# Performance work log

Measured on AMD Instinct MI355X. Metric: run time of the kernel, lower is better.

The kernel has to match this reference:

```python
import jax, jax.numpy as jnp
import numpy as np

B, N, D = 256, 64, 512        # batch, num_patches, dim
H, DH = 8, 64                 # heads, dim_head
INNER = H * DH                # 512
SCALE = DH ** -0.5


def setup_inputs() -> dict:
    key = jax.random.key(0)
    k0, k1, k2, k3, k4 = jax.random.split(key, 5)
    s = 0.02
    return {
        "x": jax.random.normal(k0, (B, N, D), jnp.float32),
        "Wq": jax.random.normal(k1, (D, INNER), jnp.float32) * s,      # to_q (no bias)
        "Wkv": jax.random.normal(k2, (D, 2 * INNER), jnp.float32) * s,  # to_k_v (no bias)
        "Wout": jax.random.normal(k3, (INNER, D), jnp.float32) * s,     # to_out Linear weight
        "bout": jnp.zeros((D,), jnp.float32),                           # to_out Linear bias
        "Wspec": jax.random.normal(k4, (N, 3 * N), jnp.float32) * s,    # to_qkv_spec (no bias)
    }


def reference(x, Wq, Wkv, Wout, bout, Wspec):
    b, n, d = x.shape
    # --- center-token spatial attention ---
    median_idx = n // 2
    x_center = jnp.broadcast_to(x[:, median_idx:median_idx + 1, :], (b, n, d))
    q = (x_center @ Wq).reshape(b, n, H, DH).transpose(0, 2, 1, 3)   # b h n dh
    kv = x @ Wkv                                                      # b n 2*inner
    k, v = jnp.split(kv, 2, axis=-1)
    k = k.reshape(b, n, H, DH).transpose(0, 2, 1, 3)                  # b h n dh
    v = v.reshape(b, n, H, DH).transpose(0, 2, 1, 3)                  # b h n dh
    attn = jax.nn.softmax(jnp.einsum('bhnd,bhmd->bhnm', q, k) * SCALE, axis=-1)
    out = jnp.einsum('bhnm,bhmd->bhnd', attn, v)                      # b h n dh
    out = out.transpose(0, 2, 1, 3).reshape(b, n, INNER)              # b n inner
    spatial_out = out @ Wout + bout                                   # b n d (dropout=0 -> identity)
    # --- transposed spectral attention ---
    x_t = x.transpose(0, 2, 1)                                        # b d n
    qkv = x_t @ Wspec                                                 # b d 3n
    q_s, k_s, _v_s = jnp.split(qkv, 3, axis=-1)                       # v_spec is unused in the original
    spec_weights = jax.nn.softmax(
        jnp.einsum('bdn,ben->bde', q_s, k_s) * SCALE, axis=-1)        # b d d
    # --- final combining matmul ---
    return jnp.einsum('bnd,bde->bne', spatial_out, spec_weights)      # b n d
```

## Files before the change

kernel.cpp:

```cpp
#include <hip/hip_runtime.h>

#define NP 64
#define DIM 512
#define NH 8
#define SCALE 0.125f

typedef __attribute__((ext_vector_type(4))) float f32x4;
typedef __attribute__((ext_vector_type(8))) short bf16x8;

#define WS_C   0
#define WS_MT  8192
#define WS_PT  4202496
#define WS_U   8396800
#define WS_Y   10493952

static __device__ __forceinline__ unsigned short f2bf(float f) {
  unsigned int u = __builtin_bit_cast(unsigned int, f);
  u += 0x7fffu + ((u >> 16) & 1u);
  return (unsigned short)(u >> 16);
}
static __device__ __forceinline__ float bf2f(unsigned short s) {
  return __builtin_bit_cast(float, ((unsigned int)s) << 16);
}
static __device__ __forceinline__ unsigned pk2(float a, float b) {
  return (unsigned)f2bf(a) | ((unsigned)f2bf(b) << 16);
}

__global__ __launch_bounds__(512)
void kw_prep(const float* __restrict__ Wq, const float* __restrict__ Wkv,
             const float* __restrict__ Wout, const float* __restrict__ Wspec,
             char* __restrict__ ws) {
  __shared__ float wa[64 * 65];
  __shared__ float wb[64 * 65];
  const int t = threadIdx.x;
  const int blk = blockIdx.x;
  const int sr = t >> 3, sc8 = (t & 7) * 8;

  if (blk == 1024) {
    #pragma unroll
    for (int cc = 0; cc < 8; ++cc) {
      wa[sr * 65 + sc8 + cc] = Wspec[sr * 192 + sc8 + cc];
      wb[sr * 65 + sc8 + cc] = Wspec[sr * 192 + 64 + sc8 + cc];
    }
    __syncthreads();
    const int m = sr, mm0 = sc8;
    float acc[8] = {0.f, 0.f, 0.f, 0.f, 0.f, 0.f, 0.f, 0.f};
    for (int n = 0; n < 64; ++n) {
      float qv = wa[m * 65 + n];
      #pragma unroll
      for (int j = 0; j < 8; ++j)
        acc[j] = fmaf(qv, wb[(mm0 + j) * 65 + n], acc[j]);
    }
    uint4 pk;
    pk.x = pk2(acc[0] * SCALE, acc[1] * SCALE);
    pk.y = pk2(acc[2] * SCALE, acc[3] * SCALE);
    pk.z = pk2(acc[4] * SCALE, acc[5] * SCALE);
    pk.w = pk2(acc[6] * SCALE, acc[7] * SCALE);
    *(uint4*)(ws + WS_C + m * 128 + ((mm0 * 2) ^ ((m & 7) << 4))) = pk;
    return;
  }

  const bool isP = blk >= 512;
  const int id = blk & 511;
  const int h = id >> 6, et = (id >> 3) & 7, dt = id & 7;

  const float* sa = isP ? (Wkv + (size_t)(dt * 64 + sr) * 1024 + 512 + h * 64)
                        : (Wq + (size_t)(dt * 64 + sr) * 512 + h * 64);
  const float* sb = isP ? (Wout + (size_t)(h * 64 + sr) * 512 + et * 64)
                        : (Wkv + (size_t)(et * 64 + sr) * 1024 + h * 64);
  {
    float4 a0 = *(const float4*)(sa + sc8), a1 = *(const float4*)(sa + sc8 + 4);
    float* d = wa + sr * 65 + sc8;
    d[0] = a0.x; d[1] = a0.y; d[2] = a0.z; d[3] = a0.w;
    d[4] = a1.x; d[5] = a1.y; d[6] = a1.z; d[7] = a1.w;
    float4 b0 = *(const float4*)(sb + sc8), b1 = *(const float4*)(sb + sc8 + 4);
    float* e = wb + sr * 65 + sc8;
    e[0] = b0.x; e[1] = b0.y; e[2] = b0.z; e[3] = b0.w;
    e[4] = b1.x; e[5] = b1.y; e[6] = b1.z; e[7] = b1.w;
  }
  __syncthreads();

  const int er = sr, dc8 = sc8;
  float acc[8] = {0.f, 0.f, 0.f, 0.f, 0.f, 0.f, 0.f, 0.f};
  if (!isP) {
    for (int j = 0; j < 64; ++j) {
      float bv = wb[er * 65 + j];
      #pragma unroll
      for (int dd = 0; dd < 8; ++dd)
        acc[dd] = fmaf(bv, wa[(dc8 + dd) * 65 + j], acc[dd]);
    }
  } else {
    for (int j = 0; j < 64; ++j) {
      float bv = wb[j * 65 + er];
      #pragma unroll
      for (int dd = 0; dd < 8; ++dd)
        acc[dd] = fmaf(bv, wa[(dc8 + dd) * 65 + j], acc[dd]);
    }
  }
  uint4 pk;
  pk.x = pk2(acc[0], acc[1]);
  pk.y = pk2(acc[2], acc[3]);
  pk.z = pk2(acc[4], acc[5]);
  pk.w = pk2(acc[6], acc[7]);
  if (!isP)
    *(uint4*)(ws + WS_MT + ((size_t)(h * 512 + et * 64 + er) * 512 + dt * 64 + dc8) * 2) = pk;
  else
    *(uint4*)(ws + WS_PT + ((size_t)(et * 64 + er) * 4096 + h * 512 + dt * 64 + dc8) * 2) = pk;
}

#define GEMM_LDS 131072
__global__ __launch_bounds__(512, 2)
void ku_u(const float* __restrict__ x, const char* __restrict__ ws,
          char* __restrict__ ws_u) {
  extern __shared__ char sm[];
  char* At = sm;
  char* Bt = sm + 65536;
  const int t = threadIdx.x, lane = t & 63, wave = t >> 6;
  const int bt = blockIdx.x >> 6, nt = blockIdx.x & 63;
  const int b0 = bt * 64, n0 = nt * 64;
  const char* Mt = ws + WS_MT;

  #pragma unroll
  for (int i = 0; i < 8; ++i) {
    const int r = wave * 8 + i;
    const float4* xr = (const float4*)(x + ((size_t)(b0 + r) * 64 + 32) * 512);
    float4 a = xr[lane], c = xr[64 + lane];
    uint2 pa = {pk2(a.x, a.y), pk2(a.z, a.w)};
    uint2 pc = {pk2(c.x, c.y), pk2(c.z, c.w)};
    const int swz = (r & 7) << 4;
    const int byt = (8 * (lane & 15)) ^ swz;
    *(uint2*)(At + (lane >> 4) * 8192 + r * 128 + byt) = pa;
    *(uint2*)(At + (4 + (lane >> 4)) * 8192 + r * 128 + byt) = pc;
  }
  #pragma unroll
  for (int i = 0; i < 8; ++i) {
    const int r = wave * 8 + i;
    uint4 v = ((const uint4*)(Mt + (size_t)(n0 + r) * 1024))[lane];
    *(uint4*)(Bt + (lane >> 3) * 8192 + r * 128 + ((16 * (lane & 7)) ^ ((r & 7) << 4))) = v;
  }
  __syncthreads();

  const int lo = ((lane & 15) * 128) + (((lane >> 4) * 16) ^ ((lane & 7) << 4));
  const int hi = ((lane & 15) * 128) + ((((lane >> 4) * 16) + 64) ^ ((lane & 7) << 4));
  const int bsub = wave & 3, npair = wave >> 2;

  f32x4 c0 = {0.f, 0.f, 0.f, 0.f}, c1 = {0.f, 0.f, 0.f, 0.f};
  #pragma unroll
  for (int kc = 0; kc < 8; ++kc) {
    const char* ab = At + kc * 8192 + bsub * 2048;
    bf16x8 aL = *(const bf16x8*)(ab + lo);
    bf16x8 aH = *(const bf16x8*)(ab + hi);
    const char* bb0 = Bt + kc * 8192 + (npair * 2) * 2048;
    const char* bb1 = bb0 + 2048;
    c0 = __builtin_amdgcn_mfma_f32_16x16x32_bf16(aL, *(const bf16x8*)(bb0 + lo), c0, 0, 0, 0);
    c0 = __builtin_amdgcn_mfma_f32_16x16x32_bf16(aH, *(const bf16x8*)(bb0 + hi), c0, 0, 0, 0);
    c1 = __builtin_amdgcn_mfma_f32_16x16x32_bf16(aL, *(const bf16x8*)(bb1 + lo), c1, 0, 0, 0);
    c1 = __builtin_amdgcn_mfma_f32_16x16x32_bf16(aH, *(const bf16x8*)(bb1 + hi), c1, 0, 0, 0);
  }
  unsigned short* U = (unsigned short*)ws_u;
  const int brow = b0 + bsub * 16 + (lane >> 4) * 4;
  const int nc0 = n0 + (npair * 2) * 16 + (lane & 15);
  #pragma unroll
  for (int r = 0; r < 4; ++r) {
    U[(size_t)(brow + r) * 4096 + nc0] = f2bf(c0[r]);
    U[(size_t)(brow + r) * 4096 + nc0 + 16] = f2bf(c1[r]);
  }
}

__global__ __launch_bounds__(512)
void k2_attn(const float* __restrict__ x, const char* __restrict__ ws_u,
             char* __restrict__ ws_y) {
  __shared__ float ul[8 * 512];
  __shared__ float scoreL[8 * 64];
  __shared__ float pT[64 * 8];
  const int t = threadIdx.x;
  const int lane = t & 63;
  const int wave = t >> 6;
  const int b = blockIdx.x;
  const float* xb = x + (size_t)b * NP * DIM;

  {
    uint4 v = ((const uint4*)(ws_u + (size_t)b * 8192))[t];
    const unsigned short* pv = (const unsigned short*)&v;
    float* d = ul + t * 8;
    #pragma unroll
    for (int g = 0; g < 8; ++g) d[g] = bf2f(pv[g]);
  }
  __syncthreads();

  {
    float4 uf0[8], uf1[8];
    #pragma unroll
    for (int h = 0; h < 8; ++h) {
      uf0[h] = *(const float4*)(ul + h * 512 + 4 * lane);
      uf1[h] = *(const float4*)(ul + h * 512 + 256 + 4 * lane);
    }
    #pragma unroll 2
    for (int i = 0; i < 8; ++i) {
      const int m = wave * 8 + i;
      const float4* xr = (const float4*)(xb + (size_t)m * DIM);
      float4 xv0 = xr[lane];
      float4 xv1 = xr[64 + lane];
      #pragma unroll
      for (int h = 0; h < 8; ++h) {
        float p = xv0.x * uf0[h].x + xv0.y * uf0[h].y + xv0.z * uf0[h].z + xv0.w * uf0[h].w
                + xv1.x * uf1[h].x + xv1.y * uf1[h].y + xv1.z * uf1[h].z + xv1.w * uf1[h].w;
        p += __shfl_xor(p, 1);
        p += __shfl_xor(p, 2);
        p += __shfl_xor(p, 4);
        p += __shfl_xor(p, 8);
        p += __shfl_xor(p, 16);
        p += __shfl_xor(p, 32);
        if (lane == 0) scoreL[h * 64 + m] = p;
      }
    }
  }
  __syncthreads();

  {
    float sc = scoreL[wave * 64 + lane] * SCALE;
    float mx = sc;
    #pragma unroll
    for (int off = 32; off > 0; off >>= 1)
      mx = fmaxf(mx, __shfl_xor(mx, off));
    float ev = __expf(sc - mx);
    float sm = ev;
    #pragma unroll
    for (int off = 32; off > 0; off >>= 1)
      sm += __shfl_xor(sm, off);
    pT[lane * NH + wave] = ev / sm;
  }
  __syncthreads();

  {
    float acc[NH];
    #pragma unroll
    for (int h = 0; h < NH; ++h) acc[h] = 0.f;
    #pragma unroll 2
    for (int m = 0; m < NP; ++m) {
      float xv = xb[(size_t)m * DIM + t];
      const float4* pp = (const float4*)(pT + m * NH);
      float4 p0 = pp[0], p1 = pp[1];
      acc[0] = fmaf(p0.x, xv, acc[0]);
      acc[1] = fmaf(p0.y, xv, acc[1]);
      acc[2] = fmaf(p0.z, xv, acc[2]);
      acc[3] = fmaf(p0.w, xv, acc[3]);
      acc[4] = fmaf(p1.x, xv, acc[4]);
      acc[5] = fmaf(p1.y, xv, acc[5]);
      acc[6] = fmaf(p1.z, xv, acc[6]);
      acc[7] = fmaf(p1.w, xv, acc[7]);
    }
    unsigned short* Y = (unsigned short*)ws_y;
    #pragma unroll
    for (int h = 0; h < NH; ++h)
      Y[(size_t)b * 4096 + h * 512 + t] = f2bf(acc[h]);
  }
}

__global__ __launch_bounds__(512, 2)
void ks_s(const char* __restrict__ ws_y, const char* __restrict__ ws_pt,
          float* __restrict__ Spart) {
  extern __shared__ char sm[];
  char* At = sm;
  char* Bt = sm + 65536;
  const int t = threadIdx.x, lane = t & 63, wave = t >> 6;
  const int bt = blockIdx.x >> 6, et = (blockIdx.x >> 3) & 7, sl = blockIdx.x & 7;
  const int b0 = bt * 64, e0 = et * 64;
  const size_t kb2 = (size_t)sl * 1024;

  #pragma unroll
  for (int i = 0; i < 8; ++i) {
    const int r = wave * 8 + i;
    const int byt = (16 * (lane & 7)) ^ ((r & 7) << 4);
    uint4 va = ((const uint4*)(ws_y + (size_t)(b0 + r) * 8192 + kb2))[lane];
    *(uint4*)(At + (lane >> 3) * 8192 + r * 128 + byt) = va;
    uint4 vb = ((const uint4*)(ws_pt + (size_t)(e0 + r) * 8192 + kb2))[lane];
    *(uint4*)(Bt + (lane >> 3) * 8192 + r * 128 + byt) = vb;
  }
  __syncthreads();

  const int lo = ((lane & 15) * 128) + (((lane >> 4) * 16) ^ ((lane & 7) << 4));
  const int hi = ((lane & 15) * 128) + ((((lane >> 4) * 16) + 64) ^ ((lane & 7) << 4));
  const int bsub = wave & 3, epair = wave >> 2;

  f32x4 c0 = {0.f, 0.f, 0.f, 0.f}, c1 = {0.f, 0.f, 0.f, 0.f};
  #pragma unroll
  for (int kc = 0; kc < 8; ++kc) {
    const char* ab = At + kc * 8192 + bsub * 2048;
    bf16x8 aL = *(const bf16x8*)(ab + lo);
    bf16x8 aH = *(const bf16x8*)(ab + hi);
    const char* bb0 = Bt + kc * 8192 + (epair * 2) * 2048;
    const char* bb1 = bb0 + 2048;
    c0 = __builtin_amdgcn_mfma_f32_16x16x32_bf16(aL, *(const bf16x8*)(bb0 + lo), c0, 0, 0, 0);
    c0 = __builtin_amdgcn_mfma_f32_16x16x32_bf16(aH, *(const bf16x8*)(bb0 + hi), c0, 0, 0, 0);
    c1 = __builtin_amdgcn_mfma_f32_16x16x32_bf16(aL, *(const bf16x8*)(bb1 + lo), c1, 0, 0, 0);
    c1 = __builtin_amdgcn_mfma_f32_16x16x32_bf16(aH, *(const bf16x8*)(bb1 + hi), c1, 0, 0, 0);
  }
  const int brow = b0 + bsub * 16 + (lane >> 4) * 4;
  const int ec0 = e0 + (epair * 2) * 16 + (lane & 15);
  #pragma unroll
  for (int r = 0; r < 4; ++r) {
    Spart[((size_t)sl * 256 + brow + r) * 512 + ec0] = c0[r];
    Spart[((size_t)sl * 256 + brow + r) * 512 + ec0 + 16] = c1[r];
  }
}

#define K4_LDS 141312
__global__ __launch_bounds__(512, 2)
void k4_spec(const float* __restrict__ x, const char* __restrict__ Cws,
             const float* __restrict__ Spart, const float* __restrict__ bout,
             float* __restrict__ out) {
  extern __shared__ char smem[];
  char* xTc = smem;
  char* w2Tc = smem + 65536;
  char* Cc = smem + 131072;
  float* s_l = (float*)(smem + 139264);

  const int t = threadIdx.x;
  const int lane = t & 63;
  const int wave = t >> 6;
  const int b = blockIdx.x;
  const float* xb = x + (size_t)b * NP * DIM;

  const int lo_off = ((lane & 15) * 128) + ((((lane >> 4) * 16)) ^ ((lane & 7) << 4));
  const int hi_off = ((lane & 15) * 128) + ((((lane >> 4) * 16) + 64) ^ ((lane & 7) << 4));

  {
    const int d = t;
    #pragma unroll
    for (int c = 0; c < 8; ++c) {
      float v0 = xb[(c * 8 + 0) * DIM + d];
      float v1 = xb[(c * 8 + 1) * DIM + d];
      float v2 = xb[(c * 8 + 2) * DIM + d];
      float v3 = xb[(c * 8 + 3) * DIM + d];
      float v4 = xb[(c * 8 + 4) * DIM + d];
      float v5 = xb[(c * 8 + 5) * DIM + d];
      float v6 = xb[(c * 8 + 6) * DIM + d];
      float v7 = xb[(c * 8 + 7) * DIM + d];
      uint4 pk;
      pk.x = pk2(v0, v1);
      pk.y = pk2(v2, v3);
      pk.z = pk2(v4, v5);
      pk.w = pk2(v6, v7);
      *(uint4*)(xTc + d * 128 + ((c * 16) ^ ((d & 7) << 4))) = pk;
    }
    ((uint4*)Cc)[t] = ((const uint4*)Cws)[t];
    float sacc = bout[t];
    #pragma unroll
    for (int sl = 0; sl < 8; ++sl)
      sacc += Spart[((size_t)sl * 256 + b) * 512 + t];
    s_l[t] = sacc;
  }
  __syncthreads();

  {
    bf16x8 af0[4], af1[4];
    #pragma unroll
    for (int mt = 0; mt < 4; ++mt) {
      af0[mt] = *(const bf16x8*)(Cc + mt * 16 * 128 + lo_off);
      af1[mt] = *(const bf16x8*)(Cc + mt * 16 * 128 + hi_off);
    }
    #pragma unroll
    for (int etl = 0; etl < 4; ++etl) {
      const int e0 = (wave * 4 + etl) * 16;
      bf16x8 b0 = *(const bf16x8*)(xTc + e0 * 128 + lo_off);
      bf16x8 b1 = *(const bf16x8*)(xTc + e0 * 128 + hi_off);
      #pragma unroll
      for (int mt = 0; mt < 4; ++mt) {
        f32x4 c = {0.f, 0.f, 0.f, 0.f};
        c = __builtin_amdgcn_mfma_f32_16x16x32_bf16(af0[mt], b0, c, 0, 0, 0);
        c = __builtin_amdgcn_mfma_f32_16x16x32_bf16(af1[mt], b1, c, 0, 0, 0);
        const int e = e0 + (lane & 15);
        const int mrow = mt * 16 + (lane >> 4) * 4;
        uint2 pk;
        pk.x = pk2(c[0], c[1]);
        pk.y = pk2(c[2], c[3]);
        *(uint2*)(w2Tc + e * 128 + ((mrow * 2) ^ ((e & 7) << 4))) = pk;
      }
    }
  }
  __syncthreads();

  float treg[32];
  #pragma unroll
  for (int et = 0; et < 32; ++et) treg[et] = 0.f;

  for (int pass = 0; pass < 4; ++pass) {
    const int d0 = pass * 128 + wave * 16;
    bf16x8 a0 = *(const bf16x8*)(xTc + d0 * 128 + lo_off);
    bf16x8 a1 = *(const bf16x8*)(xTc + d0 * 128 + hi_off);

    float rs[4] = {0.f, 0.f, 0.f, 0.f};
    #pragma unroll 4
    for (int et = 0; et < 32; ++et) {
      bf16x8 b0 = *(const bf16x8*)(w2Tc + et * 2048 + lo_off);
      bf16x8 b1 = *(const bf16x8*)(w2Tc + et * 2048 + hi_off);
      f32x4 c = {0.f, 0.f, 0.f, 0.f};
      c = __builtin_amdgcn_mfma_f32_16x16x32_bf16(a0, b0, c, 0, 0, 0);
      c = __builtin_amdgcn_mfma_f32_16x16x32_bf16(a1, b1, c, 0, 0, 0);
      rs[0] += __expf(c[0]);
      rs[1] += __expf(c[1]);
      rs[2] += __expf(c[2]);
      rs[3] += __expf(c[3]);
    }
    #pragma unroll
    for (int r = 0; r < 4; ++r) {
      rs[r] += __shfl_xor(rs[r], 1);
      rs[r] += __shfl_xor(rs[r], 2);
      rs[r] += __shfl_xor(rs[r], 4);
      rs[r] += __shfl_xor(rs[r], 8);
    }
    float coef[4];
    #pragma unroll
    for (int r = 0; r < 4; ++r)
      coef[r] = s_l[d0 + (lane >> 4) * 4 + r] / rs[r];

    #pragma unroll 4
    for (int et = 0; et < 32; ++et) {
      bf16x8 b0 = *(const bf16x8*)(w2Tc + et * 2048 + lo_off);
      bf16x8 b1 = *(const bf16x8*)(w2Tc + et * 2048 + hi_off);
      f32x4 c = {0.f, 0.f, 0.f, 0.f};
      c = __builtin_amdgcn_mfma_f32_16x16x32_bf16(a0, b0, c, 0, 0, 0);
      c = __builtin_amdgcn_mfma_f32_16x16x32_bf16(a1, b1, c, 0, 0, 0);
      float tp = treg[et];
      tp = fmaf(coef[0], __expf(c[0]), tp);
      tp = fmaf(coef[1], __expf(c[1]), tp);
      tp = fmaf(coef[2], __expf(c[2]), tp);
      tp = fmaf(coef[3], __expf(c[3]), tp);
      treg[et] = tp;
    }
  }
  __syncthreads();

  #pragma unroll
  for (int et = 0; et < 32; ++et) {
    treg[et] += __shfl_xor(treg[et], 16);
    treg[et] += __shfl_xor(treg[et], 32);
  }
  float* wpart = (float*)xTc;
  if (lane < 16) {
    #pragma unroll
    for (int et = 0; et < 32; ++et)
      wpart[wave * 512 + et * 16 + lane] = treg[et];
  }
  __syncthreads();

  float tf = 0.f;
  #pragma unroll
  for (int w = 0; w < 8; ++w) tf += wpart[w * 512 + t];

  float* ob = out + (size_t)b * NP * DIM + t;
  #pragma unroll 4
  for (int n = 0; n < NP; ++n) ob[n * DIM] = tf;
}

extern "C" void kernel_launch(void* const* d_in, const int* in_sizes, int n_in,
                              void* d_out, int out_size, void* d_ws, size_t ws_size,
                              hipStream_t stream) {
  (void)in_sizes; (void)n_in; (void)out_size; (void)ws_size;
  const float* x     = (const float*)d_in[0];
  const float* Wq    = (const float*)d_in[1];
  const float* Wkv   = (const float*)d_in[2];
  const float* Wout  = (const float*)d_in[3];
  const float* bout  = (const float*)d_in[4];
  const float* Wspec = (const float*)d_in[5];
  float* out = (float*)d_out;

  char* ws = (char*)d_ws;

  hipFuncSetAttribute(reinterpret_cast<const void*>(ku_u),
                      hipFuncAttributeMaxDynamicSharedMemorySize, GEMM_LDS);
  hipFuncSetAttribute(reinterpret_cast<const void*>(ks_s),
                      hipFuncAttributeMaxDynamicSharedMemorySize, GEMM_LDS);
  hipFuncSetAttribute(reinterpret_cast<const void*>(k4_spec),
                      hipFuncAttributeMaxDynamicSharedMemorySize, K4_LDS);

  kw_prep<<<dim3(1025), dim3(512), 0, stream>>>(Wq, Wkv, Wout, Wspec, ws);
  ku_u   <<<dim3(256),  dim3(512), GEMM_LDS, stream>>>(x, ws, ws + WS_U);
  k2_attn<<<dim3(256),  dim3(512), 0, stream>>>(x, ws + WS_U, ws + WS_Y);
  ks_s   <<<dim3(256),  dim3(512), GEMM_LDS, stream>>>(ws + WS_Y, ws + WS_PT,
                                                       (float*)(ws + WS_MT));
  k4_spec<<<dim3(256),  dim3(512), K4_LDS, stream>>>(x, ws, (const float*)(ws + WS_MT),
                                                     bout, out);
}
```

Baseline: 116.4 us.

## Cache softmax exponentials in registers instead of recomputing the spectral matmul

The spectral softmax-weighted reduction in k4 used to compute the d×e logits twice, once for the row sums and again for the weighted accumulation. Each wave now covers half of the e range, keeps its exponentials packed as bf16 in registers, and exchanges partial row sums through LDS with a barrier on every pass. This removes the second MFMA and exp sweep. In exchange it adds register pressure, since the launch bound no longer requests two blocks per CU, and it rounds the exp values to bf16 before summing.

```diff
diff --git a/kernel.cpp b/kernel.cpp
--- a/kernel.cpp
+++ b/kernel.cpp
@@ -305,16 +305,17 @@
   }
 }
 
-#define K4_LDS 141312
-__global__ __launch_bounds__(512, 2)
+#define K4_LDS 142336
+__global__ __launch_bounds__(512)
 void k4_spec(const float* __restrict__ x, const char* __restrict__ Cws,
              const float* __restrict__ Spart, const float* __restrict__ bout,
              float* __restrict__ out) {
   extern __shared__ char smem[];
-  char* xTc = smem;
+  char* xTc  = smem;
   char* w2Tc = smem + 65536;
-  char* Cc = smem + 131072;
+  char* Cc   = smem + 131072;
   float* s_l = (float*)(smem + 139264);
+  float* rsx = (float*)(smem + 141312);
 
   const int t = threadIdx.x;
   const int lane = t & 63;
@@ -365,12 +366,12 @@
       const int e0 = (wave * 4 + etl) * 16;
       bf16x8 b0 = *(const bf16x8*)(xTc + e0 * 128 + lo_off);
       bf16x8 b1 = *(const bf16x8*)(xTc + e0 * 128 + hi_off);
+      const int e = e0 + (lane & 15);
       #pragma unroll
       for (int mt = 0; mt < 4; ++mt) {
         f32x4 c = {0.f, 0.f, 0.f, 0.f};
         c = __builtin_amdgcn_mfma_f32_16x16x32_bf16(af0[mt], b0, c, 0, 0, 0);
         c = __builtin_amdgcn_mfma_f32_16x16x32_bf16(af1[mt], b1, c, 0, 0, 0);
-        const int e = e0 + (lane & 15);
         const int mrow = mt * 16 + (lane >> 4) * 4;
         uint2 pk;
         pk.x = pk2(c[0], c[1]);
@@ -381,27 +382,36 @@
   }
   __syncthreads();
 
-  float treg[32];
-  #pragma unroll
-  for (int et = 0; et < 32; ++et) treg[et] = 0.f;
-
-  for (int pass = 0; pass < 4; ++pass) {
-    const int d0 = pass * 128 + wave * 16;
+  const int dslot = wave & 3, ehalf = wave >> 2;
+  const int rowg = (lane >> 4) * 4;
+  float treg[16];
+  #pragma unroll
+  for (int i = 0; i < 16; ++i) treg[i] = 0.f;
+
+  #pragma unroll 1
+  for (int pass = 0; pass < 8; ++pass) {
+    const int d0 = (pass * 4 + dslot) * 16;
     bf16x8 a0 = *(const bf16x8*)(xTc + d0 * 128 + lo_off);
     bf16x8 a1 = *(const bf16x8*)(xTc + d0 * 128 + hi_off);
 
     float rs[4] = {0.f, 0.f, 0.f, 0.f};
-    #pragma unroll 4
-    for (int et = 0; et < 32; ++et) {
+    uint2 pex[16];
+    #pragma unroll
+    for (int i = 0; i < 16; ++i) {
+      const int et = ehalf * 16 + i;
       bf16x8 b0 = *(const bf16x8*)(w2Tc + et * 2048 + lo_off);
       bf16x8 b1 = *(const bf16x8*)(w2Tc + et * 2048 + hi_off);
       f32x4 c = {0.f, 0.f, 0.f, 0.f};
       c = __builtin_amdgcn_mfma_f32_16x16x32_bf16(a0, b0, c, 0, 0, 0);
       c = __builtin_amdgcn_mfma_f32_16x16x32_bf16(a1, b1, c, 0, 0, 0);
-      rs[0] += __expf(c[0]);
-      rs[1] += __expf(c[1]);
-      rs[2] += __expf(c[2]);
-      rs[3] += __expf(c[3]);
+      uint2 p;
+      p.x = pk2(__expf(c[0]), __expf(c[1]));
+      p.y = pk2(__expf(c[2]), __expf(c[3]));
+      pex[i] = p;
+      rs[0] += bf2f((unsigned short)(p.x & 0xffffu));
+      rs[1] += bf2f((unsigned short)(p.x >> 16));
+      rs[2] += bf2f((unsigned short)(p.y & 0xffffu));
+      rs[3] += bf2f((unsigned short)(p.y >> 16));
     }
     #pragma unroll
     for (int r = 0; r < 4; ++r) {
@@ -410,44 +420,48 @@
       rs[r] += __shfl_xor(rs[r], 4);
       rs[r] += __shfl_xor(rs[r], 8);
     }
+    const int pb = pass & 1;
+    if ((lane & 15) == 0) {
+      #pragma unroll
+      for (int r = 0; r < 4; ++r)
+        rsx[pb * 128 + wave * 16 + rowg + r] = rs[r];
+    }
+    __syncthreads();
     float coef[4];
     #pragma unroll
-    for (int r = 0; r < 4; ++r)
-      coef[r] = s_l[d0 + (lane >> 4) * 4 + r] / rs[r];
-
-    #pragma unroll 4
-    for (int et = 0; et < 32; ++et) {
-      bf16x8 b0 = *(const bf16x8*)(w2Tc + et * 2048 + lo_off);
-      bf16x8 b1 = *(const bf16x8*)(w2Tc + et * 2048 + hi_off);
-      f32x4 c = {0.f, 0.f, 0.f, 0.f};
-      c = __builtin_amdgcn_mfma_f32_16x16x32_bf16(a0, b0, c, 0, 0, 0);
-      c = __builtin_amdgcn_mfma_f32_16x16x32_bf16(a1, b1, c, 0, 0, 0);
-      float tp = treg[et];
-      tp = fmaf(coef[0], __expf(c[0]), tp);
-      tp = fmaf(coef[1], __expf(c[1]), tp);
-      tp = fmaf(coef[2], __expf(c[2]), tp);
-      tp = fmaf(coef[3], __expf(c[3]), tp);
-      treg[et] = tp;
-    }
-  }
-  __syncthreads();
-
-  #pragma unroll
-  for (int et = 0; et < 32; ++et) {
-    treg[et] += __shfl_xor(treg[et], 16);
-    treg[et] += __shfl_xor(treg[et], 32);
+    for (int r = 0; r < 4; ++r) {
+      const float rfull = rsx[pb * 128 + wave * 16 + rowg + r]
+                        + rsx[pb * 128 + (wave ^ 4) * 16 + rowg + r];
+      coef[r] = s_l[d0 + rowg + r] / rfull;
+    }
+    #pragma unroll
+    for (int i = 0; i < 16; ++i) {
+      uint2 p = pex[i];
+      float tp = treg[i];
+      tp = fmaf(coef[0], bf2f((unsigned short)(p.x & 0xffffu)), tp);
+      tp = fmaf(coef[1], bf2f((unsigned short)(p.x >> 16)), tp);
+      tp = fmaf(coef[2], bf2f((unsigned short)(p.y & 0xffffu)), tp);
+      tp = fmaf(coef[3], bf2f((unsigned short)(p.y >> 16)), tp);
+      treg[i] = tp;
+    }
+  }
+
+  #pragma unroll
+  for (int i = 0; i < 16; ++i) {
+    treg[i] += __shfl_xor(treg[i], 16);
+    treg[i] += __shfl_xor(treg[i], 32);
   }
   float* wpart = (float*)xTc;
   if (lane < 16) {
     #pragma unroll
-    for (int et = 0; et < 32; ++et)
-      wpart[wave * 512 + et * 16 + lane] = treg[et];
+    for (int i = 0; i < 16; ++i)
+      wpart[dslot * 512 + ehalf * 256 + i * 16 + lane] = treg[i];
   }
   __syncthreads();
 
   float tf = 0.f;
   #pragma unroll
-  for (int w = 0; w < 8; ++w) tf += wpart[w * 512 + t];
+  for (int w = 0; w < 4; ++w) tf += wpart[w * 512 + t];
 
   float* ob = out + (size_t)b * NP * DIM + t;
   #pragma unroll 4
```

After: 108.0 us (median of 3 runs). -7.3%, faster.
